# Kernel optimization log

Measured on AMD Instinct MI355X. Metric: run time of the kernel, lower is better.

The kernel has to match this reference:

```python
import jax, jax.numpy as jnp
import numpy as np

# skeletal graph constants
CONN_A = np.array([0,1,2,0,4,5,0,7,8,0,10,11,0,13,14])
CONN_B = np.array([1,2,3,4,5,6,7,8,9,10,11,12,13,14,15])
# angle-limited joints with their (parent, child) from the connection lists
ANG_J = np.array([11,14,5,8]); ANG_P = np.array([10,13,4,7]); ANG_C = np.array([12,15,6,9])


def setup_inputs() -> dict:
    key = jax.random.key(0)
    ks = jax.random.split(key, 16)
    B, T, J, C = 64, 243, 17, 128
    def lin(k, fin, fout):
        kw, kb = jax.random.split(k)
        s = 1.0 / np.sqrt(fin)
        return (jax.random.uniform(kw, (fin, fout), jnp.float32, -s, s),
                jax.random.uniform(kb, (fout,), jnp.float32, -s, s))
    aw1, ab1 = lin(ks[0], C, C // 2)
    aw2, ab2 = lin(ks[1], C // 2, 3)
    bw1, bb1 = lin(ks[2], 2 * C, C)
    bw2, bb2 = lin(ks[3], C, 1)
    cw1, cb1 = lin(ks[4], C * J, 64)
    cw2, cb2 = lin(ks[5], 64, 8)
    return {
        "features": jax.random.normal(ks[6], (B, T, J, C), jnp.float32),
        "pose3d": jax.random.normal(ks[7], (B, T, J, 3), jnp.float32),
        "aw1": aw1, "ab1": ab1, "aw2": aw2, "ab2": ab2,
        "bw1": bw1, "bb1": bb1, "bw2": bw2, "bb2": bb2,
        "cw1": cw1, "cb1": cb1, "cw2": cw2, "cb2": cb2,
    }


def _gelu(x):
    return jax.nn.gelu(x, approximate=False)


def reference(features, pose3d, aw1, ab1, aw2, ab2, bw1, bb1, bw2, bb2, cw1, cb1, cw2, cb2):
    B, T, J, C = features.shape
    # angle predictor: Linear -> GELU -> Linear on every joint feature
    predicted_angles = _gelu(features @ aw1 + ab1) @ aw2 + ab2  # [B,T,J,3]

    # actual bone lengths: vectorized gather over 15 connections
    vec = pose3d[:, :, CONN_B, :] - pose3d[:, :, CONN_A, :]       # [B,T,15,3]
    actual_bone_lengths = jnp.linalg.norm(vec, axis=-1, keepdims=True)  # [B,T,15,1]

    # bone features: concat endpoint features, small MLP
    bone_feat = jnp.concatenate([features[:, :, CONN_A, :], features[:, :, CONN_B, :]], axis=-1)  # [B,T,15,2C]
    predicted_bone_lengths = jax.nn.relu(_gelu(bone_feat @ bw1 + bb1) @ bw2 + bb2)  # [B,T,15,1]

    # actual joint angles at the 4 angle-limited joints, zeros elsewhere
    v1 = pose3d[:, :, ANG_J, :] - pose3d[:, :, ANG_P, :]
    v2 = pose3d[:, :, ANG_C, :] - pose3d[:, :, ANG_J, :]
    v1 = v1 / (jnp.linalg.norm(v1, axis=-1, keepdims=True) + 1e-10)
    v2 = v2 / (jnp.linalg.norm(v2, axis=-1, keepdims=True) + 1e-10)
    dot = jnp.clip(jnp.sum(v1 * v2, axis=-1, keepdims=True), -1 + 1e-7, 1 - 1e-7)
    angle = jnp.arccos(dot)  # [B,T,4,1]
    actual_angles = jnp.zeros((B, T, J, 1), features.dtype).at[:, :, ANG_J, :].set(angle)

    # action classifier on time-averaged flattened joint features
    action_feat = features.reshape(B, T, J * C).mean(axis=1)  # [B,J*C]
    action_logits = _gelu(action_feat @ cw1 + cb1) @ cw2 + cb2  # [B,8]

    return (predicted_angles, actual_angles, predicted_bone_lengths, actual_bone_lengths, action_logits)
```

## Files before the change

kernel.cpp:

```cpp
#include <hip/hip_runtime.h>
#include <math.h>

#define NF 15552
#define NJ 17
#define NC 128
#define JC (NJ*NC)

constexpr int cA[15] = {0,1,2,0,4,5,0,7,8,0,10,11,0,13,14};
constexpr int cB[15] = {1,2,3,4,5,6,7,8,9,10,11,12,13,14,15};
constexpr int aJ[4] = {11,14,5,8};
constexpr int aP[4] = {10,13,4,7};
constexpr int aCc[4] = {12,15,6,9};

__device__ const int d_cA16[16] = {0,1,2,0,4,5,0,7,8,0,10,11,0,13,14,0};
__device__ const int d_cB16[16] = {1,2,3,4,5,6,7,8,9,10,11,12,13,14,15,0};

typedef __bf16 bf16x8 __attribute__((ext_vector_type(8)));
typedef float f32x4 __attribute__((ext_vector_type(4)));
typedef unsigned short u16x8 __attribute__((ext_vector_type(8)));
typedef unsigned short u16x4 __attribute__((ext_vector_type(4)));

__device__ __forceinline__ float gelu_exact(float x){
  return 0.5f * x * (1.0f + erff(x * 0.7071067811865476f));
}

__device__ __forceinline__ unsigned short f2bf(float f){
  unsigned u = __builtin_bit_cast(unsigned, f);
  unsigned r = (u + 0x7FFFu + ((u >> 16) & 1u)) >> 16;
  return (unsigned short)r;
}

__global__ __launch_bounds__(256) void k_geom(const float* __restrict__ pose,
                                              float* __restrict__ out_aa,
                                              float* __restrict__ out_abl)
{
  const int f = blockIdx.x * 256 + threadIdx.x;
  if (f >= NF) return;
  const float* p = pose + (long)f * NJ * 3;
  float px[NJ], py[NJ], pz[NJ];
  #pragma unroll
  for (int j = 0; j < NJ; ++j){ px[j] = p[3*j]; py[j] = p[3*j+1]; pz[j] = p[3*j+2]; }

  #pragma unroll
  for (int i = 0; i < 15; ++i){
    const int a = cA[i], b = cB[i];
    const float dx = px[b]-px[a], dy = py[b]-py[a], dz = pz[b]-pz[a];
    out_abl[(long)f*15 + i] = sqrtf(dx*dx + dy*dy + dz*dz);
  }

  float ang[NJ];
  #pragma unroll
  for (int j = 0; j < NJ; ++j) ang[j] = 0.0f;
  #pragma unroll
  for (int i = 0; i < 4; ++i){
    const int jj = aJ[i], pp = aP[i], cc = aCc[i];
    float v1x = px[jj]-px[pp], v1y = py[jj]-py[pp], v1z = pz[jj]-pz[pp];
    float v2x = px[cc]-px[jj], v2y = py[cc]-py[jj], v2z = pz[cc]-pz[jj];
    const float n1 = sqrtf(v1x*v1x + v1y*v1y + v1z*v1z) + 1e-10f;
    const float n2 = sqrtf(v2x*v2x + v2y*v2y + v2z*v2z) + 1e-10f;
    v1x /= n1; v1y /= n1; v1z /= n1;
    v2x /= n2; v2y /= n2; v2z /= n2;
    float d = v1x*v2x + v1y*v2y + v1z*v2z;
    d = fminf(fmaxf(d, -1.0f + 1e-7f), 1.0f - 1e-7f);
    ang[jj] = acosf(d);
  }
  #pragma unroll
  for (int j = 0; j < NJ; ++j) out_aa[(long)f*NJ + j] = ang[j];
}

#define AITERS 3
#define AROWS_PER_BLOCK (64*AITERS)
#define ASTRIDE 136

__global__ __launch_bounds__(256) void k_angle_mfma(const float* __restrict__ feat,
    const float* __restrict__ aw1, const float* __restrict__ ab1,
    const float* __restrict__ aw2, const float* __restrict__ ab2,
    float* __restrict__ out_pa)
{
  __shared__ __align__(16) unsigned short s_a[2][64][ASTRIDE];

  const int tid  = threadIdx.x;
  const int w    = tid >> 6;
  const int lane = tid & 63;
  const int g    = lane >> 4;
  const int c    = lane & 15;
  const long row0 = (long)blockIdx.x * AROWS_PER_BLOCK;

  bf16x8 bfrag[4][4];
  float b1[4], w2c[4][3];
  #pragma unroll
  for (int nf = 0; nf < 4; ++nf){
    const int col = nf*16 + c;
    b1[nf] = ab1[col];
    #pragma unroll
    for (int m = 0; m < 3; ++m) w2c[nf][m] = aw2[col*3 + m];
    #pragma unroll
    for (int kt = 0; kt < 4; ++kt){
      u16x8 t;
      #pragma unroll
      for (int e = 0; e < 8; ++e)
        t[e] = f2bf(aw1[(kt*32 + g*8 + e)*64 + col]);
      bfrag[kt][nf] = __builtin_bit_cast(bf16x8, t);
    }
  }
  const float b2[3] = {ab2[0], ab2[1], ab2[2]};

  auto stage = [&](int buf, int it){
    const float* src = feat + (row0 + (long)it*64) * NC;
    unsigned short* dst = &s_a[buf][0][0];
    #pragma unroll
    for (int u0 = 0; u0 < 2048; u0 += 256){
      const int u = u0 + tid;
      const int r = u >> 5, e4 = (u & 31) << 2;
      const float4 v = *(const float4*)(src + r*NC + e4);
      u16x4 p; p[0]=f2bf(v.x); p[1]=f2bf(v.y); p[2]=f2bf(v.z); p[3]=f2bf(v.w);
      *(u16x4*)(dst + r*ASTRIDE + e4) = p;
    }
  };

  stage(0, 0);
  int buf = 0;

  for (int it = 0; it < AITERS; ++it){
    __syncthreads();
    if (it + 1 < AITERS) stage(buf ^ 1, it + 1);

    f32x4 acc[4];
    #pragma unroll
    for (int nf = 0; nf < 4; ++nf) acc[nf] = (f32x4)0.0f;

    const unsigned short* ab = &s_a[buf][0][0];
    const int arow = w*16 + c;
    #pragma unroll
    for (int kt = 0; kt < 4; ++kt){
      const bf16x8 av = __builtin_bit_cast(bf16x8,
          *(const u16x8*)(ab + arow*ASTRIDE + kt*32 + g*8));
      #pragma unroll
      for (int nf = 0; nf < 4; ++nf)
        acc[nf] = __builtin_amdgcn_mfma_f32_16x16x32_bf16(av, bfrag[kt][nf], acc[nf], 0, 0, 0);
    }

    float s[4][3];
    #pragma unroll
    for (int r = 0; r < 4; ++r){ s[r][0]=0.f; s[r][1]=0.f; s[r][2]=0.f; }
    #pragma unroll
    for (int nf = 0; nf < 4; ++nf){
      #pragma unroll
      for (int r = 0; r < 4; ++r){
        const float h = gelu_exact(acc[nf][r] + b1[nf]);
        s[r][0] = fmaf(h, w2c[nf][0], s[r][0]);
        s[r][1] = fmaf(h, w2c[nf][1], s[r][1]);
        s[r][2] = fmaf(h, w2c[nf][2], s[r][2]);
      }
    }
    #pragma unroll
    for (int r = 0; r < 4; ++r){
      #pragma unroll
      for (int m = 0; m < 3; ++m){
        float v = s[r][m];
        v += __shfl_xor(v, 1);
        v += __shfl_xor(v, 2);
        v += __shfl_xor(v, 4);
        v += __shfl_xor(v, 8);
        s[r][m] = v;
      }
    }
    if (c == 0){
      const long grow = row0 + (long)it*64 + w*16 + g*4;
      #pragma unroll
      for (int r = 0; r < 4; ++r){
        #pragma unroll
        for (int m = 0; m < 3; ++m)
          out_pa[(grow + r)*3 + m] = s[r][m] + b2[m];
      }
    }
    buf ^= 1;
  }
}

#define BFPI 4
#define BITERS 2
#define BFB (BFPI*BITERS)
#define FSTRIDE 136
#define FELEMS (NJ*FSTRIDE)

__global__ __launch_bounds__(256) void k_bone_mfma(const float* __restrict__ feat,
    const float* __restrict__ bw1, const float* __restrict__ bb1,
    const float* __restrict__ bw2, const float* __restrict__ bb2,
    float* __restrict__ out_pbl)
{
  __shared__ __align__(16) unsigned short s_feat[2][BFPI][NJ][FSTRIDE];
  __shared__ float s_red[4][BFPI][16];

  const int tid  = threadIdx.x;
  const int w    = tid >> 6;
  const int lane = tid & 63;
  const int g    = lane >> 4;
  const int c    = lane & 15;
  const long f0  = (long)blockIdx.x * BFB;

  bf16x8 bfrag[8][2];
  float b1c[2], w2c[2];
  #pragma unroll
  for (int nf = 0; nf < 2; ++nf){
    const int col = w*32 + nf*16 + c;
    b1c[nf] = bb1[col];
    w2c[nf] = bw2[col];
    #pragma unroll
    for (int ks = 0; ks < 8; ++ks){
      u16x8 t;
      #pragma unroll
      for (int e = 0; e < 8; ++e)
        t[e] = f2bf(bw1[(ks*32 + g*8 + e)*128 + col]);
      bfrag[ks][nf] = __builtin_bit_cast(bf16x8, t);
    }
  }

  const int jA = d_cA16[c], jB = d_cB16[c];
  int aoff[8];
  #pragma unroll
  for (int ks = 0; ks < 8; ++ks){
    const int kk = ks*32 + g*8;
    aoff[ks] = (kk < 128) ? (jA*FSTRIDE + kk) : (jB*FSTRIDE + (kk - 128));
  }

  auto stage = [&](int buf, int it){
    unsigned short* dst = &s_feat[buf][0][0][0];
    const float* src = feat + (f0 + (long)it*BFPI) * JC;
    for (int u = tid; u < BFPI*544; u += 256){
      const int fi = u / 544, rem = u - fi*544;
      const int joint = rem >> 5, e4 = (rem & 31) << 2;
      const float4 v = *(const float4*)(src + (long)fi*JC + joint*128 + e4);
      u16x4 p; p[0]=f2bf(v.x); p[1]=f2bf(v.y); p[2]=f2bf(v.z); p[3]=f2bf(v.w);
      *(u16x4*)(dst + fi*FELEMS + joint*FSTRIDE + e4) = p;
    }
  };

  stage(0, 0);
  int buf = 0;

  for (int it = 0; it < BITERS; ++it){
    __syncthreads();
    if (it + 1 < BITERS) stage(buf ^ 1, it + 1);

    f32x4 acc[BFPI][2];
    #pragma unroll
    for (int fi = 0; fi < BFPI; ++fi){ acc[fi][0] = (f32x4)0.0f; acc[fi][1] = (f32x4)0.0f; }

    const unsigned short* fb = &s_feat[buf][0][0][0];
    #pragma unroll
    for (int ks = 0; ks < 8; ++ks){
      bf16x8 av[BFPI];
      #pragma unroll
      for (int fi = 0; fi < BFPI; ++fi)
        av[fi] = __builtin_bit_cast(bf16x8, *(const u16x8*)(fb + fi*FELEMS + aoff[ks]));
      #pragma unroll
      for (int fi = 0; fi < BFPI; ++fi){
        acc[fi][0] = __builtin_amdgcn_mfma_f32_16x16x32_bf16(av[fi], bfrag[ks][0], acc[fi][0], 0, 0, 0);
        acc[fi][1] = __builtin_amdgcn_mfma_f32_16x16x32_bf16(av[fi], bfrag[ks][1], acc[fi][1], 0, 0, 0);
      }
    }

    #pragma unroll
    for (int fi = 0; fi < BFPI; ++fi){
      float s[4] = {0.f, 0.f, 0.f, 0.f};
      #pragma unroll
      for (int nf = 0; nf < 2; ++nf){
        #pragma unroll
        for (int r = 0; r < 4; ++r)
          s[r] += gelu_exact(acc[fi][nf][r] + b1c[nf]) * w2c[nf];
      }
      #pragma unroll
      for (int r = 0; r < 4; ++r){
        s[r] += __shfl_xor(s[r], 1);
        s[r] += __shfl_xor(s[r], 2);
        s[r] += __shfl_xor(s[r], 4);
        s[r] += __shfl_xor(s[r], 8);
      }
      if (c == 0){
        #pragma unroll
        for (int r = 0; r < 4; ++r) s_red[w][fi][g*4 + r] = s[r];
      }
    }
    __syncthreads();
    if (tid < BFPI*15){
      const int fi = tid / 15, row = tid - fi*15;
      const float v = s_red[0][fi][row] + s_red[1][fi][row] +
                      s_red[2][fi][row] + s_red[3][fi][row] + bb2[0];
      out_pbl[(f0 + (long)it*BFPI + fi)*15 + row] = fmaxf(v, 0.0f);
    }
    buf ^= 1;
  }
}

__global__ __launch_bounds__(256) void k_mean(const float* __restrict__ feat,
                                              float* __restrict__ mean_ws)
{
  const int jc = blockIdx.x * 256 + threadIdx.x;
  const int b = blockIdx.y;
  if (jc >= JC) return;
  float s = 0.0f;
  const float* p = feat + (long)b * 243 * JC + jc;
  #pragma unroll 8
  for (int t = 0; t < 243; ++t) s += p[(long)t * JC];
  mean_ws[(long)b*JC + jc] = s * (1.0f/243.0f);
}

__global__ __launch_bounds__(256) void k_action(const float* __restrict__ mean_src,
    const float* __restrict__ cw1, const float* __restrict__ cb1,
    const float* __restrict__ cw2, const float* __restrict__ cb2,
    float* __restrict__ out_lg)
{
  __shared__ float s_m[JC];
  __shared__ float s_part[4][64];
  __shared__ float s_h[64];
  const int b = blockIdx.x, tid = threadIdx.x;
  for (int i = tid; i < JC; i += 256) s_m[i] = mean_src[(long)b*JC + i];
  __syncthreads();
  const int n = tid & 63, part = tid >> 6;
  float s = 0.0f;
  const int k0 = part * 544;
  for (int k = k0; k < k0 + 544; ++k) s = fmaf(s_m[k], cw1[(long)k*64 + n], s);
  s_part[part][n] = s;
  __syncthreads();
  if (tid < 64) s_h[tid] = gelu_exact(s_part[0][tid] + s_part[1][tid] +
                                      s_part[2][tid] + s_part[3][tid] + cb1[tid]);
  __syncthreads();
  if (tid < 8){
    float v = cb2[tid];
    #pragma unroll
    for (int k = 0; k < 64; ++k) v = fmaf(s_h[k], cw2[k*8 + tid], v);
    out_lg[b*8 + tid] = v;
  }
}

extern "C" void kernel_launch(void* const* d_in, const int* in_sizes, int n_in,
                              void* d_out, int out_size, void* d_ws, size_t ws_size,
                              hipStream_t stream)
{
  const float* feat = (const float*)d_in[0];
  const float* pose = (const float*)d_in[1];
  const float* aw1  = (const float*)d_in[2];
  const float* ab1  = (const float*)d_in[3];
  const float* aw2  = (const float*)d_in[4];
  const float* ab2  = (const float*)d_in[5];
  const float* bw1  = (const float*)d_in[6];
  const float* bb1  = (const float*)d_in[7];
  const float* bw2  = (const float*)d_in[8];
  const float* bb2  = (const float*)d_in[9];
  const float* cw1  = (const float*)d_in[10];
  const float* cb1  = (const float*)d_in[11];
  const float* cw2  = (const float*)d_in[12];
  const float* cb2  = (const float*)d_in[13];

  float* out = (float*)d_out;
  float* out_pa  = out;
  float* out_aa  = out + 793152;
  float* out_pbl = out + 1057536;
  float* out_abl = out + 1290816;
  float* out_lg  = out + 1524096;

  k_geom<<<dim3((NF + 255)/256), dim3(256), 0, stream>>>(pose, out_aa, out_abl);
  k_angle_mfma<<<dim3((NF*NJ)/AROWS_PER_BLOCK), dim3(256), 0, stream>>>(feat, aw1, ab1, aw2, ab2, out_pa);
  k_bone_mfma<<<dim3(NF/BFB), dim3(256), 0, stream>>>(feat, bw1, bb1, bw2, bb2, out_pbl);

  float* mean_ws = (float*)d_ws;
  k_mean<<<dim3((JC + 255)/256, 64), dim3(256), 0, stream>>>(feat, mean_ws);
  k_action<<<dim3(64), dim3(256), 0, stream>>>(mean_ws, cw1, cb1, cw2, cb2, out_lg);
}
```

Measured before the change: 169.8 us.

## Fuse angle, bone and mean kernels into one pass over features

Merges the angle MLP, bone MLP and time-mean reduction into a single kernel. Each block stages 8 frames of features into LDS once as bf16 with an XOR swizzle, then runs both MFMA MLPs and accumulates per-batch sums with atomics. This removes the three separate reads of the large feature tensor. It also swaps exact erf GELU for an exp2/rcp sigmoid approximation and computes the mean from bf16-rounded values, which adds accuracy risk, plus atomic contention and an extra memset.

```diff
diff --git a/kernel.cpp b/kernel.cpp
--- a/kernel.cpp
+++ b/kernel.cpp
@@ -5,6 +5,8 @@
 #define NJ 17
 #define NC 128
 #define JC (NJ*NC)
+#define TT 243
+#define FB 8
 
 constexpr int cA[15] = {0,1,2,0,4,5,0,7,8,0,10,11,0,13,14};
 constexpr int cB[15] = {1,2,3,4,5,6,7,8,9,10,11,12,13,14,15};
@@ -18,16 +20,21 @@
 typedef __bf16 bf16x8 __attribute__((ext_vector_type(8)));
 typedef float f32x4 __attribute__((ext_vector_type(4)));
 typedef unsigned short u16x8 __attribute__((ext_vector_type(8)));
-typedef unsigned short u16x4 __attribute__((ext_vector_type(4)));
 
 __device__ __forceinline__ float gelu_exact(float x){
   return 0.5f * x * (1.0f + erff(x * 0.7071067811865476f));
 }
-
-__device__ __forceinline__ unsigned short f2bf(float f){
-  unsigned u = __builtin_bit_cast(unsigned, f);
-  unsigned r = (u + 0x7FFFu + ((u >> 16) & 1u)) >> 16;
-  return (unsigned short)r;
+__device__ __forceinline__ float gelu_fast(float x){
+  const float s2 = x * x;
+  const float q  = fmaf(s2, -0.1029437f, -2.3021183f);
+  const float e  = __builtin_amdgcn_exp2f(q * x);
+  return x * __builtin_amdgcn_rcpf(1.0f + e);
+}
+__device__ __forceinline__ unsigned short bfc(float x){
+  return __builtin_bit_cast(unsigned short, (__bf16)x);
+}
+__device__ __forceinline__ float bf2f(unsigned short u){
+  return __builtin_bit_cast(float, ((unsigned)u) << 16);
 }
 
 __global__ __launch_bounds__(256) void k_geom(const float* __restrict__ pose,
@@ -68,93 +75,167 @@
   for (int j = 0; j < NJ; ++j) out_aa[(long)f*NJ + j] = ang[j];
 }
 
-#define AITERS 3
-#define AROWS_PER_BLOCK (64*AITERS)
-#define ASTRIDE 136
-
-__global__ __launch_bounds__(256) void k_angle_mfma(const float* __restrict__ feat,
+#define SFO(fi, off16) (((fi)*272 + (off16))*8)
+
+__global__ __launch_bounds__(256) void k_fused(const float* __restrict__ feat,
     const float* __restrict__ aw1, const float* __restrict__ ab1,
     const float* __restrict__ aw2, const float* __restrict__ ab2,
-    float* __restrict__ out_pa)
+    const float* __restrict__ bw1, const float* __restrict__ bb1,
+    const float* __restrict__ bw2, const float* __restrict__ bb2,
+    float* __restrict__ out_pa, float* __restrict__ out_pbl,
+    float* __restrict__ mean_acc)
 {
-  __shared__ __align__(16) unsigned short s_a[2][64][ASTRIDE];
+  __shared__ __align__(16) unsigned short s_feat[FB*NJ*NC];
+  __shared__ float s_red[4][FB][16];
 
   const int tid  = threadIdx.x;
   const int w    = tid >> 6;
   const int lane = tid & 63;
   const int g    = lane >> 4;
   const int c    = lane & 15;
-  const long row0 = (long)blockIdx.x * AROWS_PER_BLOCK;
-
-  bf16x8 bfrag[4][4];
-  float b1[4], w2c[4][3];
+  const long f0  = (long)blockIdx.x * FB;
+
+  {
+    const float* base = feat + f0 * JC;
+    for (int u = tid; u < FB*272; u += 256){
+      const float4 v0 = *(const float4*)(base + u*8);
+      const float4 v1 = *(const float4*)(base + u*8 + 4);
+      u16x8 p;
+      p[0]=bfc(v0.x); p[1]=bfc(v0.y); p[2]=bfc(v0.z); p[3]=bfc(v0.w);
+      p[4]=bfc(v1.x); p[5]=bfc(v1.y); p[6]=bfc(v1.z); p[7]=bfc(v1.w);
+      const int fi = u / 272, r = u - fi*272;
+      const int j = r >> 4, kb = r & 15;
+      *(u16x8*)&s_feat[SFO(fi, j*16 + (kb ^ (j & 7)))] = p;
+    }
+  }
+
+  bf16x8 wb[8][2];
+  float bb1c[2], bw2c[2];
+  #pragma unroll
+  for (int nf = 0; nf < 2; ++nf){
+    const int col = w*32 + nf*16 + c;
+    bb1c[nf] = bb1[col];
+    bw2c[nf] = bw2[col];
+    #pragma unroll
+    for (int ks = 0; ks < 8; ++ks){
+      u16x8 t;
+      #pragma unroll
+      for (int e = 0; e < 8; ++e) t[e] = bfc(bw1[(ks*32 + g*8 + e)*128 + col]);
+      wb[ks][nf] = __builtin_bit_cast(bf16x8, t);
+    }
+  }
+
+  const int jA = d_cA16[c], jB = d_cB16[c];
+  int boff[8];
+  #pragma unroll
+  for (int ks = 0; ks < 8; ++ks){
+    const int kk = ks*32 + g*8;
+    const int j  = (kk < 128) ? jA : jB;
+    const int kb = (kk < 128) ? (ks*4 + g) : (ks*4 + g - 16);
+    boff[ks] = j*16 + (kb ^ (j & 7));
+  }
+
+  __syncthreads();
+
+  f32x4 bacc[FB][2];
+  #pragma unroll
+  for (int fi = 0; fi < FB; ++fi){ bacc[fi][0] = (f32x4)0.0f; bacc[fi][1] = (f32x4)0.0f; }
+
+  #pragma unroll
+  for (int ks = 0; ks < 8; ++ks){
+    bf16x8 av[FB];
+    #pragma unroll
+    for (int fi = 0; fi < FB; ++fi)
+      av[fi] = __builtin_bit_cast(bf16x8, *(const u16x8*)&s_feat[SFO(fi, boff[ks])]);
+    #pragma unroll
+    for (int fi = 0; fi < FB; ++fi){
+      bacc[fi][0] = __builtin_amdgcn_mfma_f32_16x16x32_bf16(av[fi], wb[ks][0], bacc[fi][0], 0, 0, 0);
+      bacc[fi][1] = __builtin_amdgcn_mfma_f32_16x16x32_bf16(av[fi], wb[ks][1], bacc[fi][1], 0, 0, 0);
+    }
+  }
+
+  #pragma unroll
+  for (int fi = 0; fi < FB; ++fi){
+    float s[4] = {0.f, 0.f, 0.f, 0.f};
+    #pragma unroll
+    for (int nf = 0; nf < 2; ++nf)
+      #pragma unroll
+      for (int r = 0; r < 4; ++r)
+        s[r] += gelu_fast(bacc[fi][nf][r] + bb1c[nf]) * bw2c[nf];
+    #pragma unroll
+    for (int r = 0; r < 4; ++r){
+      s[r] += __shfl_xor(s[r], 1);
+      s[r] += __shfl_xor(s[r], 2);
+      s[r] += __shfl_xor(s[r], 4);
+      s[r] += __shfl_xor(s[r], 8);
+    }
+    if (c == 0)
+      #pragma unroll
+      for (int r = 0; r < 4; ++r) s_red[w][fi][g*4 + r] = s[r];
+  }
+
+  bf16x8 wa[4][4];
+  float ab1c[4], aw2c[4][3];
   #pragma unroll
   for (int nf = 0; nf < 4; ++nf){
     const int col = nf*16 + c;
-    b1[nf] = ab1[col];
-    #pragma unroll
-    for (int m = 0; m < 3; ++m) w2c[nf][m] = aw2[col*3 + m];
+    ab1c[nf] = ab1[col];
+    #pragma unroll
+    for (int m = 0; m < 3; ++m) aw2c[nf][m] = aw2[col*3 + m];
     #pragma unroll
     for (int kt = 0; kt < 4; ++kt){
       u16x8 t;
       #pragma unroll
-      for (int e = 0; e < 8; ++e)
-        t[e] = f2bf(aw1[(kt*32 + g*8 + e)*64 + col]);
-      bfrag[kt][nf] = __builtin_bit_cast(bf16x8, t);
-    }
-  }
-  const float b2[3] = {ab2[0], ab2[1], ab2[2]};
-
-  auto stage = [&](int buf, int it){
-    const float* src = feat + (row0 + (long)it*64) * NC;
-    unsigned short* dst = &s_a[buf][0][0];
-    #pragma unroll
-    for (int u0 = 0; u0 < 2048; u0 += 256){
-      const int u = u0 + tid;
-      const int r = u >> 5, e4 = (u & 31) << 2;
-      const float4 v = *(const float4*)(src + r*NC + e4);
-      u16x4 p; p[0]=f2bf(v.x); p[1]=f2bf(v.y); p[2]=f2bf(v.z); p[3]=f2bf(v.w);
-      *(u16x4*)(dst + r*ASTRIDE + e4) = p;
-    }
-  };
-
-  stage(0, 0);
-  int buf = 0;
-
-  for (int it = 0; it < AITERS; ++it){
-    __syncthreads();
-    if (it + 1 < AITERS) stage(buf ^ 1, it + 1);
-
-    f32x4 acc[4];
-    #pragma unroll
-    for (int nf = 0; nf < 4; ++nf) acc[nf] = (f32x4)0.0f;
-
-    const unsigned short* ab = &s_a[buf][0][0];
-    const int arow = w*16 + c;
-    #pragma unroll
-    for (int kt = 0; kt < 4; ++kt){
-      const bf16x8 av = __builtin_bit_cast(bf16x8,
-          *(const u16x8*)(ab + arow*ASTRIDE + kt*32 + g*8));
+      for (int e = 0; e < 8; ++e) t[e] = bfc(aw1[(kt*32 + g*8 + e)*64 + col]);
+      wa[kt][nf] = __builtin_bit_cast(bf16x8, t);
+    }
+  }
+  const float ab2c[3] = {ab2[0], ab2[1], ab2[2]};
+
+  const int fa0 = 2*w, fa1 = 2*w + 1;
+  f32x4 acc0[4], acc1[4], accj[4];
+  #pragma unroll
+  for (int nf = 0; nf < 4; ++nf){ acc0[nf]=(f32x4)0.0f; acc1[nf]=(f32x4)0.0f; accj[nf]=(f32x4)0.0f; }
+
+  #pragma unroll
+  for (int kt = 0; kt < 4; ++kt){
+    const int kbx = kt*4 + g;
+    const bf16x8 av0 = __builtin_bit_cast(bf16x8,
+        *(const u16x8*)&s_feat[SFO(fa0, c*16 + (kbx ^ (c & 7)))]);
+    const bf16x8 av1 = __builtin_bit_cast(bf16x8,
+        *(const u16x8*)&s_feat[SFO(fa1, c*16 + (kbx ^ (c & 7)))]);
+    #pragma unroll
+    for (int nf = 0; nf < 4; ++nf){
+      acc0[nf] = __builtin_amdgcn_mfma_f32_16x16x32_bf16(av0, wa[kt][nf], acc0[nf], 0, 0, 0);
+      acc1[nf] = __builtin_amdgcn_mfma_f32_16x16x32_bf16(av1, wa[kt][nf], acc1[nf], 0, 0, 0);
+    }
+    if (w == 0){
+      const bf16x8 avj = __builtin_bit_cast(bf16x8,
+          *(const u16x8*)&s_feat[SFO(c & 7, 16*16 + kbx)]);
       #pragma unroll
       for (int nf = 0; nf < 4; ++nf)
-        acc[nf] = __builtin_amdgcn_mfma_f32_16x16x32_bf16(av, bfrag[kt][nf], acc[nf], 0, 0, 0);
-    }
-
+        accj[nf] = __builtin_amdgcn_mfma_f32_16x16x32_bf16(avj, wa[kt][nf], accj[nf], 0, 0, 0);
+    }
+  }
+
+  #pragma unroll
+  for (int half = 0; half < 2; ++half){
+    const int fa = half ? fa1 : fa0;
+    f32x4* acc = half ? acc1 : acc0;
     float s[4][3];
     #pragma unroll
     for (int r = 0; r < 4; ++r){ s[r][0]=0.f; s[r][1]=0.f; s[r][2]=0.f; }
     #pragma unroll
-    for (int nf = 0; nf < 4; ++nf){
+    for (int nf = 0; nf < 4; ++nf)
       #pragma unroll
       for (int r = 0; r < 4; ++r){
-        const float h = gelu_exact(acc[nf][r] + b1[nf]);
-        s[r][0] = fmaf(h, w2c[nf][0], s[r][0]);
-        s[r][1] = fmaf(h, w2c[nf][1], s[r][1]);
-        s[r][2] = fmaf(h, w2c[nf][2], s[r][2]);
-      }
-    }
-    #pragma unroll
-    for (int r = 0; r < 4; ++r){
+        const float h = gelu_fast(acc[nf][r] + ab1c[nf]);
+        s[r][0] = fmaf(h, aw2c[nf][0], s[r][0]);
+        s[r][1] = fmaf(h, aw2c[nf][1], s[r][1]);
+        s[r][2] = fmaf(h, aw2c[nf][2], s[r][2]);
+      }
+    #pragma unroll
+    for (int r = 0; r < 4; ++r)
       #pragma unroll
       for (int m = 0; m < 3; ++m){
         float v = s[r][m];
@@ -164,149 +245,80 @@
         v += __shfl_xor(v, 8);
         s[r][m] = v;
       }
-    }
     if (c == 0){
-      const long grow = row0 + (long)it*64 + w*16 + g*4;
       #pragma unroll
       for (int r = 0; r < 4; ++r){
+        const long joint = g*4 + r;
         #pragma unroll
         for (int m = 0; m < 3; ++m)
-          out_pa[(grow + r)*3 + m] = s[r][m] + b2[m];
-      }
-    }
-    buf ^= 1;
-  }
-}
-
-#define BFPI 4
-#define BITERS 2
-#define BFB (BFPI*BITERS)
-#define FSTRIDE 136
-#define FELEMS (NJ*FSTRIDE)
-
-__global__ __launch_bounds__(256) void k_bone_mfma(const float* __restrict__ feat,
-    const float* __restrict__ bw1, const float* __restrict__ bb1,
-    const float* __restrict__ bw2, const float* __restrict__ bb2,
-    float* __restrict__ out_pbl)
-{
-  __shared__ __align__(16) unsigned short s_feat[2][BFPI][NJ][FSTRIDE];
-  __shared__ float s_red[4][BFPI][16];
-
-  const int tid  = threadIdx.x;
-  const int w    = tid >> 6;
-  const int lane = tid & 63;
-  const int g    = lane >> 4;
-  const int c    = lane & 15;
-  const long f0  = (long)blockIdx.x * BFB;
-
-  bf16x8 bfrag[8][2];
-  float b1c[2], w2c[2];
-  #pragma unroll
-  for (int nf = 0; nf < 2; ++nf){
-    const int col = w*32 + nf*16 + c;
-    b1c[nf] = bb1[col];
-    w2c[nf] = bw2[col];
-    #pragma unroll
-    for (int ks = 0; ks < 8; ++ks){
-      u16x8 t;
-      #pragma unroll
-      for (int e = 0; e < 8; ++e)
-        t[e] = f2bf(bw1[(ks*32 + g*8 + e)*128 + col]);
-      bfrag[ks][nf] = __builtin_bit_cast(bf16x8, t);
-    }
-  }
-
-  const int jA = d_cA16[c], jB = d_cB16[c];
-  int aoff[8];
-  #pragma unroll
-  for (int ks = 0; ks < 8; ++ks){
-    const int kk = ks*32 + g*8;
-    aoff[ks] = (kk < 128) ? (jA*FSTRIDE + kk) : (jB*FSTRIDE + (kk - 128));
-  }
-
-  auto stage = [&](int buf, int it){
-    unsigned short* dst = &s_feat[buf][0][0][0];
-    const float* src = feat + (f0 + (long)it*BFPI) * JC;
-    for (int u = tid; u < BFPI*544; u += 256){
-      const int fi = u / 544, rem = u - fi*544;
-      const int joint = rem >> 5, e4 = (rem & 31) << 2;
-      const float4 v = *(const float4*)(src + (long)fi*JC + joint*128 + e4);
-      u16x4 p; p[0]=f2bf(v.x); p[1]=f2bf(v.y); p[2]=f2bf(v.z); p[3]=f2bf(v.w);
-      *(u16x4*)(dst + fi*FELEMS + joint*FSTRIDE + e4) = p;
-    }
-  };
-
-  stage(0, 0);
-  int buf = 0;
-
-  for (int it = 0; it < BITERS; ++it){
-    __syncthreads();
-    if (it + 1 < BITERS) stage(buf ^ 1, it + 1);
-
-    f32x4 acc[BFPI][2];
-    #pragma unroll
-    for (int fi = 0; fi < BFPI; ++fi){ acc[fi][0] = (f32x4)0.0f; acc[fi][1] = (f32x4)0.0f; }
-
-    const unsigned short* fb = &s_feat[buf][0][0][0];
-    #pragma unroll
-    for (int ks = 0; ks < 8; ++ks){
-      bf16x8 av[BFPI];
-      #pragma unroll
-      for (int fi = 0; fi < BFPI; ++fi)
-        av[fi] = __builtin_bit_cast(bf16x8, *(const u16x8*)(fb + fi*FELEMS + aoff[ks]));
-      #pragma unroll
-      for (int fi = 0; fi < BFPI; ++fi){
-        acc[fi][0] = __builtin_amdgcn_mfma_f32_16x16x32_bf16(av[fi], bfrag[ks][0], acc[fi][0], 0, 0, 0);
-        acc[fi][1] = __builtin_amdgcn_mfma_f32_16x16x32_bf16(av[fi], bfrag[ks][1], acc[fi][1], 0, 0, 0);
-      }
-    }
-
-    #pragma unroll
-    for (int fi = 0; fi < BFPI; ++fi){
-      float s[4] = {0.f, 0.f, 0.f, 0.f};
-      #pragma unroll
-      for (int nf = 0; nf < 2; ++nf){
+          out_pa[((f0 + fa)*NJ + joint)*3 + m] = s[r][m] + ab2c[m];
+      }
+    }
+  }
+  if (w == 0){
+    float s[4][3];
+    #pragma unroll
+    for (int r = 0; r < 4; ++r){ s[r][0]=0.f; s[r][1]=0.f; s[r][2]=0.f; }
+    #pragma unroll
+    for (int nf = 0; nf < 4; ++nf)
+      #pragma unroll
+      for (int r = 0; r < 4; ++r){
+        const float h = gelu_fast(accj[nf][r] + ab1c[nf]);
+        s[r][0] = fmaf(h, aw2c[nf][0], s[r][0]);
+        s[r][1] = fmaf(h, aw2c[nf][1], s[r][1]);
+        s[r][2] = fmaf(h, aw2c[nf][2], s[r][2]);
+      }
+    #pragma unroll
+    for (int r = 0; r < 4; ++r)
+      #pragma unroll
+      for (int m = 0; m < 3; ++m){
+        float v = s[r][m];
+        v += __shfl_xor(v, 1);
+        v += __shfl_xor(v, 2);
+        v += __shfl_xor(v, 4);
+        v += __shfl_xor(v, 8);
+        s[r][m] = v;
+      }
+    if (c == 0 && g < 2){
+      #pragma unroll
+      for (int r = 0; r < 4; ++r){
+        const long frame = g*4 + r;
         #pragma unroll
-        for (int r = 0; r < 4; ++r)
-          s[r] += gelu_exact(acc[fi][nf][r] + b1c[nf]) * w2c[nf];
-      }
-      #pragma unroll
-      for (int r = 0; r < 4; ++r){
-        s[r] += __shfl_xor(s[r], 1);
-        s[r] += __shfl_xor(s[r], 2);
-        s[r] += __shfl_xor(s[r], 4);
-        s[r] += __shfl_xor(s[r], 8);
-      }
-      if (c == 0){
-        #pragma unroll
-        for (int r = 0; r < 4; ++r) s_red[w][fi][g*4 + r] = s[r];
-      }
-    }
-    __syncthreads();
-    if (tid < BFPI*15){
-      const int fi = tid / 15, row = tid - fi*15;
-      const float v = s_red[0][fi][row] + s_red[1][fi][row] +
-                      s_red[2][fi][row] + s_red[3][fi][row] + bb2[0];
-      out_pbl[(f0 + (long)it*BFPI + fi)*15 + row] = fmaxf(v, 0.0f);
-    }
-    buf ^= 1;
-  }
-}
-
-__global__ __launch_bounds__(256) void k_mean(const float* __restrict__ feat,
-                                              float* __restrict__ mean_ws)
-{
-  const int jc = blockIdx.x * 256 + threadIdx.x;
-  const int b = blockIdx.y;
-  if (jc >= JC) return;
-  float s = 0.0f;
-  const float* p = feat + (long)b * 243 * JC + jc;
-  #pragma unroll 8
-  for (int t = 0; t < 243; ++t) s += p[(long)t * JC];
-  mean_ws[(long)b*JC + jc] = s * (1.0f/243.0f);
-}
-
-__global__ __launch_bounds__(256) void k_action(const float* __restrict__ mean_src,
+        for (int m = 0; m < 3; ++m)
+          out_pa[((f0 + frame)*NJ + 16)*3 + m] = s[r][m] + ab2c[m];
+      }
+    }
+  }
+
+  __syncthreads();
+
+  if (tid < FB*15){
+    const int fi = tid / 15, row = tid - fi*15;
+    const float v = s_red[0][fi][row] + s_red[1][fi][row] +
+                    s_red[2][fi][row] + s_red[3][fi][row] + bb2[0];
+    out_pbl[(f0 + fi)*15 + row] = fmaxf(v, 0.0f);
+  }
+
+  {
+    const int b0 = (int)(f0 / TT);
+    const int b1 = (int)((f0 + FB - 1) / TT);
+    const int split = (b1 > b0) ? (b1*TT - (int)f0) : FB;
+    for (int jc = tid; jc < JC; jc += 256){
+      const int j = jc >> 7, k = jc & 127;
+      const int eoff = (j*16 + ((k >> 3) ^ (j & 7)))*8 + (k & 7);
+      float s0 = 0.f, s1 = 0.f;
+      #pragma unroll
+      for (int fi = 0; fi < FB; ++fi){
+        const float v = bf2f(s_feat[fi*JC + eoff]);
+        if (fi < split) s0 += v; else s1 += v;
+      }
+      atomicAdd(&mean_acc[(long)b0*JC + jc], s0);
+      if (b1 > b0) atomicAdd(&mean_acc[(long)b1*JC + jc], s1);
+    }
+  }
+}
+
+__global__ __launch_bounds__(256) void k_action(const float* __restrict__ sum_src,
     const float* __restrict__ cw1, const float* __restrict__ cb1,
     const float* __restrict__ cw2, const float* __restrict__ cb2,
     float* __restrict__ out_lg)
@@ -315,7 +327,7 @@
   __shared__ float s_part[4][64];
   __shared__ float s_h[64];
   const int b = blockIdx.x, tid = threadIdx.x;
-  for (int i = tid; i < JC; i += 256) s_m[i] = mean_src[(long)b*JC + i];
+  for (int i = tid; i < JC; i += 256) s_m[i] = sum_src[(long)b*JC + i] * (1.0f/243.0f);
   __syncthreads();
   const int n = tid & 63, part = tid >> 6;
   float s = 0.0f;
@@ -360,11 +372,12 @@
   float* out_abl = out + 1290816;
   float* out_lg  = out + 1524096;
 
+  float* mean_acc = (float*)d_ws;
+  hipMemsetAsync(mean_acc, 0, (size_t)64 * JC * sizeof(float), stream);
+
   k_geom<<<dim3((NF + 255)/256), dim3(256), 0, stream>>>(pose, out_aa, out_abl);
-  k_angle_mfma<<<dim3((NF*NJ)/AROWS_PER_BLOCK), dim3(256), 0, stream>>>(feat, aw1, ab1, aw2, ab2, out_pa);
-  k_bone_mfma<<<dim3(NF/BFB), dim3(256), 0, stream>>>(feat, bw1, bb1, bw2, bb2, out_pbl);
-
-  float* mean_ws = (float*)d_ws;
-  k_mean<<<dim3((JC + 255)/256, 64), dim3(256), 0, stream>>>(feat, mean_ws);
-  k_action<<<dim3(64), dim3(256), 0, stream>>>(mean_ws, cw1, cb1, cw2, cb2, out_lg);
-}
+  k_fused<<<dim3(NF/FB), dim3(256), 0, stream>>>(feat, aw1, ab1, aw2, ab2,
+                                                 bw1, bb1, bw2, bb2,
+                                                 out_pa, out_pbl, mean_acc);
+  k_action<<<dim3(64), dim3(256), 0, stream>>>(mean_acc, cw1, cb1, cw2, cb2, out_lg);
+}
```

Result: faster. 146.9 us (-13.5%).
